# Optimization experiments

Hardware: AMD Instinct MI355X
Metric: run time of the kernel (lower is better)

Reference implementation:

```python
import jax, jax.numpy as jnp
import numpy as np

H = 8            # num_heads
DK = 256         # head_qk_dim
DV = 512         # head_v_dim
EPS = 1e-5
ROPE_BASE = 10000.0


def _rope(x):
    # x: [B, T, H, DK]; GPT-NeoX style (non-interleaved halves), seqlen_offset=0
    B, T, h, d = x.shape
    inv_freq = 1.0 / (ROPE_BASE ** (jnp.arange(0, d, 2, dtype=jnp.float32) / d))  # [d/2]
    t = jnp.arange(T, dtype=jnp.float32)
    freqs = t[:, None] * inv_freq[None, :]              # [T, d/2]
    cos = jnp.cos(freqs)[None, :, None, :]              # [1, T, 1, d/2]
    sin = jnp.sin(freqs)[None, :, None, :]
    x1, x2 = x[..., : d // 2], x[..., d // 2 :]
    return jnp.concatenate([x1 * cos - x2 * sin, x2 * cos + x1 * sin], axis=-1)


def setup_inputs() -> dict:
    key = jax.random.key(0)
    ks = jax.random.split(key, 7)
    hidden = 2048
    B, T = 2, 2048
    w = 0.02
    return {
        "hidden_states": jax.random.normal(ks[0], (B, T, hidden), jnp.float32),
        "Wq": jax.random.normal(ks[1], (hidden, H * DK), jnp.float32) * w,
        "Wk": jax.random.normal(ks[2], (hidden, H * DK), jnp.float32) * w,
        "Wv": jax.random.normal(ks[3], (hidden, H * DV), jnp.float32) * w,
        "Wg": jax.random.normal(ks[4], (hidden, H * DV), jnp.float32) * w,
        "Wo": jax.random.normal(ks[5], (H * DV, hidden), jnp.float32) * w,
        "g_norm_weight": jnp.ones((DV,), jnp.float32),
    }


def reference(hidden_states, Wq, Wk, Wv, Wg, Wo, g_norm_weight):
    B, T, _ = hidden_states.shape
    q = (hidden_states @ Wq).reshape(B, T, H, DK)
    k = (hidden_states @ Wk).reshape(B, T, H, DK)
    v = (hidden_states @ Wv).reshape(B, T, H, DV)
    g = (hidden_states @ Wg).reshape(B, T, H, DV)

    q = _rope(q)
    k = _rope(k)

    # per-head RetNet decay: gamma_h = 1 - 2^(-5-h)
    gamma = 1.0 - jnp.exp2(-5.0 - jnp.arange(H, dtype=jnp.float32))     # [H]
    idx = jnp.arange(T)
    diff = idx[:, None] - idx[None, :]                                   # [T, T]
    causal = diff >= 0
    log2g = jnp.log2(gamma)[:, None, None]                               # [H,1,1]
    D = jnp.where(causal[None], jnp.exp2(log2g * jnp.where(causal, diff, 0)[None]), 0.0)  # [H,T,T]

    scale = DK ** -0.5
    scores = jnp.einsum("bihd,bjhd->bhij", q * scale, k) * D[None]       # [B,H,T,T]
    o = jnp.einsum("bhij,bjhd->bihd", scores, v)                          # [B,T,H,DV]

    # fused RMSNorm (per head over DV) + swish gate
    rms = jax.lax.rsqrt(jnp.mean(o * o, axis=-1, keepdims=True) + EPS)
    o = o * rms * g_norm_weight
    o = o * (g * jax.nn.sigmoid(g))

    return o.reshape(B, T, H * DV) @ Wo
```

## Files before the change

### kernel.cpp

```cpp
#include <hip/hip_runtime.h>
#include <hip/hip_bf16.h>
#include <math.h>

#define NH 8
#define DKk 256
#define DVv 512
#define Bn 2
#define Tn 2048
#define HID 2048
#define EPSf 1e-5f

typedef __bf16 bf16x8 __attribute__((ext_vector_type(8)));
typedef float f32x4 __attribute__((ext_vector_type(4)));
typedef unsigned short us8 __attribute__((ext_vector_type(8)));
using bf16 = __hip_bfloat16;
typedef unsigned short ushort_t;

__device__ __forceinline__ void gload_lds16(const void* g, void* lds_base) {
  __builtin_amdgcn_global_load_lds(
      (const __attribute__((address_space(1))) void*)g,
      (__attribute__((address_space(3))) void*)lds_base, 16, 0, 0);
}

__device__ __forceinline__ ushort_t f2bf_raw(float f) {
  bf16 h = __float2bfloat16(f);
  return *reinterpret_cast<ushort_t*>(&h);
}
__device__ __forceinline__ float bf2f_raw(ushort_t u) {
  union { unsigned int i; float f; } v; v.i = ((unsigned int)u) << 16; return v.f;
}

__global__ void k_f32_to_bf16(const float4* __restrict__ in, ushort4* __restrict__ out, int n4) {
  int i = blockIdx.x * blockDim.x + threadIdx.x;
  if (i >= n4) return;
  float4 v = in[i];
  ushort4 o;
  o.x = f2bf_raw(v.x); o.y = f2bf_raw(v.y); o.z = f2bf_raw(v.z); o.w = f2bf_raw(v.w);
  out[i] = o;
}

__global__ void k_add2_f32(const float4* __restrict__ a, const float4* __restrict__ b,
                           float4* __restrict__ o, int n4) {
  int i = blockIdx.x * blockDim.x + threadIdx.x;
  if (i >= n4) return;
  float4 x = a[i], y = b[i];
  float4 r; r.x = x.x + y.x; r.y = x.y + y.y; r.z = x.z + y.z; r.w = x.w + y.w;
  o[i] = r;
}

__global__ __launch_bounds__(256) void k_transpose64(const float* __restrict__ W, bf16* __restrict__ WT,
                                                     int K, int N) {
  __shared__ unsigned int t32[64 * 33];
  const int tid = threadIdx.x;
  const int n0 = blockIdx.x * 64, k0 = blockIdx.y * 64;
  const int a = tid >> 3;
  const int bq = tid & 7;

  const float* r0 = W + (size_t)(k0 + 2 * a) * N + n0 + bq * 8;
  const float* r1 = r0 + N;
  float4 v00 = *(const float4*)r0;
  float4 v01 = *(const float4*)(r0 + 4);
  float4 v10 = *(const float4*)r1;
  float4 v11 = *(const float4*)(r1 + 4);
  float e0[8] = {v00.x, v00.y, v00.z, v00.w, v01.x, v01.y, v01.z, v01.w};
  float e1[8] = {v10.x, v10.y, v10.z, v10.w, v11.x, v11.y, v11.z, v11.w};
#pragma unroll
  for (int j = 0; j < 8; j++) {
    unsigned int val = (unsigned int)f2bf_raw(e0[j]) | ((unsigned int)f2bf_raw(e1[j]) << 16);
    t32[(bq * 8 + j) * 33 + a] = val;
  }
  __syncthreads();
  const int nl = tid >> 2, part = tid & 3;
  unsigned int c[8];
#pragma unroll
  for (int i = 0; i < 8; i++) c[i] = t32[nl * 33 + part * 8 + i];
  char* dst = (char*)(WT + (size_t)(n0 + nl) * K + k0 + part * 16);
  uint4 lo; lo.x = c[0]; lo.y = c[1]; lo.z = c[2]; lo.w = c[3];
  uint4 hi; hi.x = c[4]; hi.y = c[5]; hi.z = c[6]; hi.w = c[7];
  *(uint4*)dst = lo;
  *(uint4*)(dst + 16) = hi;
}

#define BARX() asm volatile("s_barrier" ::: "memory")
#define LGKM0() { asm volatile("s_waitcnt lgkmcnt(0)" ::: "memory"); __builtin_amdgcn_sched_barrier(0); }
#define VMW4() asm volatile("s_waitcnt vmcnt(4)" ::: "memory")
#define VMW0() asm volatile("s_waitcnt vmcnt(0)" ::: "memory")
#define PRIO1 __builtin_amdgcn_s_setprio(1)
#define PRIO0 __builtin_amdgcn_s_setprio(0)

#define QUADQ(MB, NB)                                                              \
  { _Pragma("unroll") for (int kk_ = 0; kk_ < 2; ++kk_)                            \
    _Pragma("unroll") for (int mf_ = 0; mf_ < 4; ++mf_)                            \
    _Pragma("unroll") for (int nf_ = 0; nf_ < 2; ++nf_)                            \
      acc[(MB) + mf_][(NB) + nf_] = __builtin_amdgcn_mfma_f32_16x16x32_bf16(       \
          ar[(MB) + mf_][kk_], br[(NB) + nf_][kk_],                                \
          acc[(MB) + mf_][(NB) + nf_], 0, 0, 0); }

template <int MODE>
__global__ __launch_bounds__(512, 2) void k_gemm8(const bf16* __restrict__ A, const bf16* __restrict__ BT,
                                                  void* __restrict__ O0, void* __restrict__ O1,
                                                  int nsplit, int M, int Ntot, int Kloop, int Kstride) {
  extern __shared__ char lds[];
  const int tid = threadIdx.x;
  const int lane = tid & 63;
  const int w = tid >> 6;
  const int wr = w >> 2;
  const int wc = w & 3;
  const int quad = lane >> 4, c16 = lane & 15;
  const int m0 = blockIdx.y * 256, n0 = blockIdx.x * 256;
  const int ks = blockIdx.z;

  const bf16* Ab = A + (size_t)ks * Kloop;
  const bf16* Bb = BT + (size_t)ks * Kloop;

  const int srow = (w << 4) | (lane >> 3);
  const int gsw = (((lane & 7) ^ (lane >> 3)) << 4);
  const size_t rowBytes = (size_t)Kstride * 2;
  const char* aS = (const char*)(Ab + (size_t)(m0 + srow) * Kstride) + gsw;
  const char* bS = (const char*)(Bb + (size_t)(n0 + srow) * Kstride) + gsw;

  auto stage = [&](int matB, int buf, int h, int t) {
    const char* base = (matB ? bS : aS) + (size_t)h * 128 * rowBytes + (size_t)t * 128;
    char* ldst = lds + buf * 65536 + matB * 32768 + h * 16384 + w * 2048;
    gload_lds16(base, ldst);
    gload_lds16(base + 8 * rowBytes, ldst + 1024);
  };
  auto ldA = [&](int buf, int mf, int kk) -> bf16x8 {
    int row = wr * 128 + mf * 16 + c16;
    return *(const bf16x8*)(lds + buf * 65536 + row * 128 + ((((kk << 2) | quad) ^ (c16 & 7)) << 4));
  };
  auto ldB = [&](int buf, int nf, int kk) -> bf16x8 {
    int row = wc * 64 + nf * 16 + c16;
    return *(const bf16x8*)(lds + buf * 65536 + 32768 + row * 128 + ((((kk << 2) | quad) ^ (c16 & 7)) << 4));
  };

  f32x4 acc[8][4];
  const f32x4 fz = {0.f, 0.f, 0.f, 0.f};
#pragma unroll
  for (int i = 0; i < 8; i++)
#pragma unroll
    for (int j = 0; j < 4; j++) acc[i][j] = fz;
  bf16x8 ar[8][2], br[4][2];

  const int nT = Kloop >> 6;
  const int nIter = nT >> 1;

  stage(0, 0, 0, 0); stage(0, 0, 1, 0);
  stage(1, 0, 0, 0); stage(1, 0, 1, 0);
  stage(0, 1, 0, 1); stage(0, 1, 1, 1);
  VMW4();
  BARX();

  for (int it = 0; it < nIter; ++it) {
    const int t = it * 2;
    const bool last = (it == nIter - 1);
#pragma unroll
    for (int mf = 0; mf < 4; ++mf) { ar[mf][0] = ldA(0, mf, 0); ar[mf][1] = ldA(0, mf, 1); }
#pragma unroll
    for (int nf = 0; nf < 2; ++nf) { br[nf][0] = ldB(0, nf, 0); br[nf][1] = ldB(0, nf, 1); }
    stage(1, 1, 0, t + 1);
    BARX(); LGKM0();
    PRIO1; QUADQ(0, 0); PRIO0;
    BARX();
#pragma unroll
    for (int mf = 4; mf < 8; ++mf) { ar[mf][0] = ldA(0, mf, 0); ar[mf][1] = ldA(0, mf, 1); }
    stage(1, 1, 1, t + 1);
    BARX(); LGKM0();
    PRIO1; QUADQ(4, 0); PRIO0;
    BARX();
#pragma unroll
    for (int nf = 2; nf < 4; ++nf) { br[nf][0] = ldB(0, nf, 0); br[nf][1] = ldB(0, nf, 1); }
    if (!last) stage(0, 0, 0, t + 2);
    BARX(); LGKM0();
    PRIO1; QUADQ(0, 2); PRIO0;
    BARX();
    if (!last) stage(0, 0, 1, t + 2);
    BARX();
    PRIO1; QUADQ(4, 2); PRIO0;
    if (!last) { VMW4(); } else { VMW0(); }
    BARX();
#pragma unroll
    for (int mf = 0; mf < 4; ++mf) { ar[mf][0] = ldA(1, mf, 0); ar[mf][1] = ldA(1, mf, 1); }
#pragma unroll
    for (int nf = 0; nf < 2; ++nf) { br[nf][0] = ldB(1, nf, 0); br[nf][1] = ldB(1, nf, 1); }
    if (!last) stage(1, 0, 0, t + 2);
    BARX(); LGKM0();
    PRIO1; QUADQ(0, 0); PRIO0;
    BARX();
#pragma unroll
    for (int mf = 4; mf < 8; ++mf) { ar[mf][0] = ldA(1, mf, 0); ar[mf][1] = ldA(1, mf, 1); }
    if (!last) stage(1, 0, 1, t + 2);
    BARX(); LGKM0();
    PRIO1; QUADQ(4, 0); PRIO0;
    BARX();
#pragma unroll
    for (int nf = 2; nf < 4; ++nf) { br[nf][0] = ldB(1, nf, 0); br[nf][1] = ldB(1, nf, 1); }
    if (!last) stage(0, 1, 0, t + 3);
    BARX(); LGKM0();
    PRIO1; QUADQ(0, 2); PRIO0;
    BARX();
    if (!last) stage(0, 1, 1, t + 3);
    BARX();
    PRIO1; QUADQ(4, 2); PRIO0;
    if (!last) VMW4();
    BARX();
  }

  if (MODE == 2) {
    __syncthreads();
    ushort_t* tile = (ushort_t*)lds;
#pragma unroll
    for (int mf = 0; mf < 8; ++mf)
#pragma unroll
      for (int nf = 0; nf < 4; ++nf)
#pragma unroll
        for (int rr = 0; rr < 4; ++rr) {
          int row = wr * 128 + mf * 16 + quad * 4 + rr;
          int col = wc * 64 + nf * 16 + c16;
          tile[row * 256 + col] = f2bf_raw(acc[mf][nf][rr]);
        }
    __syncthreads();
    const bool qside = (n0 < nsplit);
    bf16* Ob = (bf16*)(qside ? O0 : O1);
    const float scale = qside ? 0.0625f : 1.0f;
    const int h = (qside ? n0 : n0 - nsplit) >> 8;
#pragma unroll
    for (int j = 0; j < 8; ++j) {
      int u = j * 512 + tid;
      int row = u >> 4;
      int ch = u & 15;
      const ushort_t* lp = tile + row * 256 + ch * 8;
      us8 lo = *(const us8*)lp;
      us8 hi = *(const us8*)(lp + 128);
      int m = m0 + row;
      float tf = (float)(m & (Tn - 1));
      us8 olo, ohi;
#pragma unroll
      for (int e = 0; e < 8; ++e) {
        int i = ch * 8 + e;
        float inv = exp2f(-(float)i * (13.287712379549449f / 128.0f));
        float ang = tf * inv;
        float s, c;
        sincosf(ang, &s, &c);
        float x1 = bf2f_raw(lo[e]);
        float x2 = bf2f_raw(hi[e]);
        olo[e] = f2bf_raw((x1 * c - x2 * s) * scale);
        ohi[e] = f2bf_raw((x2 * c + x1 * s) * scale);
      }
      ushort_t* dst = (ushort_t*)Ob + ((size_t)m * NH + h) * DKk + ch * 8;
      *(us8*)dst = olo;
      *(us8*)(dst + 128) = ohi;
    }
  } else if (MODE == 1) {
    float* Ob = (float*)(ks ? O1 : O0);
#pragma unroll
    for (int mf = 0; mf < 8; ++mf)
#pragma unroll
      for (int nf = 0; nf < 4; ++nf)
#pragma unroll
        for (int rr = 0; rr < 4; ++rr) {
          int m = m0 + wr * 128 + mf * 16 + quad * 4 + rr;
          int n = n0 + wc * 64 + nf * 16 + c16;
          Ob[(size_t)m * Ntot + n] = acc[mf][nf][rr];
        }
  } else if (MODE == 3 && n0 < nsplit) {
    __syncthreads();
    ushort_t* tile = (ushort_t*)lds;
#pragma unroll
    for (int mf = 0; mf < 8; ++mf)
#pragma unroll
      for (int nf = 0; nf < 4; ++nf)
#pragma unroll
        for (int rr = 0; rr < 4; ++rr) {
          int row = wr * 128 + mf * 16 + quad * 4 + rr;
          int col = wc * 64 + nf * 16 + c16;
          tile[row * 256 + col] = f2bf_raw(acc[mf][nf][rr]);
        }
    __syncthreads();
    const int b = m0 >> 11;
    const int kt0 = (m0 & 2047) >> 5;
    const int h = n0 >> 9;
    const int dv0 = n0 & 511;
    const int bh = b * 8 + h;
    ushort_t* vSo = (ushort_t*)O0;
#pragma unroll
    for (int uu = 0; uu < 16; ++uu) {
      int u = uu * 512 + tid;
      int ktl = u >> 10;
      int chunk = (u >> 8) & 3;
      int dvl = u & 255;
      us8 o;
#pragma unroll
      for (int jj = 0; jj < 8; ++jj)
        o[jj] = tile[(ktl * 32 + chunk * 8 + jj) * 256 + dvl];
      *(us8*)(vSo + ((size_t)(bh * 64 + kt0 + ktl) * 2048 + chunk * 512 + (dv0 + dvl)) * 8) = o;
    }
  } else {
    bf16* Ob; int ldo, nc0;
    if (n0 < nsplit) { Ob = (bf16*)O0; ldo = nsplit; nc0 = n0; }
    else             { Ob = (bf16*)O1; ldo = Ntot - nsplit; nc0 = n0 - nsplit; }
#pragma unroll
    for (int mf = 0; mf < 8; ++mf)
#pragma unroll
      for (int nf = 0; nf < 4; ++nf)
#pragma unroll
        for (int rr = 0; rr < 4; ++rr) {
          int m = m0 + wr * 128 + mf * 16 + quad * 4 + rr;
          int n = nc0 + wc * 64 + nf * 16 + c16;
          Ob[(size_t)m * ldo + n] = __float2bfloat16(acc[mf][nf][rr]);
        }
  }
}

__global__ __launch_bounds__(256, 2) void k_retention(const bf16* __restrict__ q, const bf16* __restrict__ k,
                                                      const char* __restrict__ vS, const bf16* __restrict__ g,
                                                      const float* __restrict__ gnw, bf16* __restrict__ X) {
  extern __shared__ char smem[];
  ushort_t* p_lds_base = (ushort_t*)(smem + 65536);
  float* red = (float*)(smem + 75776);
  bf16* o_lds = (bf16*)smem;

  const int tid = threadIdx.x;
  const int l = tid & 63, w = tid >> 6;
  const int quad = l >> 4, c16 = l & 15;

  const int bid = blockIdx.x;
  const int u = (bid & 255) >> 4;
  const int qt = (bid < 256) ? (31 - u) : u;
  const int bh = bid & 15;
  const int b = bh >> 3, h = bh & 7;
  const int q0 = qt * 64;

  bf16x8 qf[8];
  {
    const bf16* qrow = q + ((size_t)(b * Tn + q0 + w * 16 + c16) * NH + h) * DKk + quad * 8;
#pragma unroll
    for (int c = 0; c < 8; c++) qf[c] = *(const bf16x8*)(qrow + c * 32);
  }

  const float log2g = log2f(1.0f - exp2f(-5.0f - (float)h));

  f32x4 acc[4][8];
  const f32x4 fz = {0.f, 0.f, 0.f, 0.f};
#pragma unroll
  for (int rt = 0; rt < 4; rt++)
#pragma unroll
    for (int n = 0; n < 8; n++) acc[rt][n] = fz;

  const int ktmax = 2 * qt + 1;
  const float Dcut = 30.0f / (-log2g);
  int kt0 = (int)fmaxf(0.0f, floorf(((float)q0 - Dcut) * (1.0f / 32.0f)));

  const char* vS_tilebase = vS + (size_t)(bh * 64) * 32768;

  auto stageK = [&](int kt) {
    const int pb = (kt - kt0) & 1;
#pragma unroll
    for (int i = 0; i < 4; i++) {
      int instr = w * 4 + i;
      int j = instr * 2 + (l >> 5);
      int cg = (l & 31) ^ (j & 7);
      const char* gp = (const char*)(k + ((size_t)(b * Tn + kt * 32 + j) * NH + h) * DKk) + cg * 16;
      gload_lds16(gp, smem + pb * 16384 + instr * 1024);
    }
  };
  auto stageV = [&](int kt) {
#pragma unroll
    for (int i = 0; i < 8; i++) {
      int instr = w * 8 + i;
      const char* gp = vS_tilebase + (size_t)kt * 32768 + instr * 1024 + l * 16;
      gload_lds16(gp, smem + 32768 + instr * 1024);
    }
  };

  auto S_phase = [&](int kt) {
    const int pb = (kt - kt0) & 1;
    f32x4 sacc[2] = {fz, fz};
#pragma unroll
    for (int jt = 0; jt < 2; jt++)
#pragma unroll
      for (int c = 0; c < 8; c++) {
        const char* kp = smem + pb * 16384 + (jt * 16 + c16) * 512 + (((c * 4 + quad) ^ (c16 & 7)) * 16);
        bf16x8 bfrag = *(const bf16x8*)kp;
        sacc[jt] = __builtin_amdgcn_mfma_f32_16x16x32_bf16(qf[c], bfrag, sacc[jt], 0, 0, 0);
      }
    ushort_t* pbuf = p_lds_base + pb * 2560;
#pragma unroll
    for (int jt = 0; jt < 2; jt++)
#pragma unroll
      for (int r = 0; r < 4; r++) {
        int ig = q0 + w * 16 + quad * 4 + r;
        int jg = kt * 32 + jt * 16 + c16;
        int d = ig - jg;
        float val = (d >= 0) ? sacc[jt][r] * exp2f(log2g * (float)d) : 0.0f;
        pbuf[(w * 16 + quad * 4 + r) * 40 + jt * 16 + c16] = f2bf_raw(val);
      }
  };

  auto PV_phase = [&](int kt) {
    const int pb = (kt - kt0) & 1;
    const char* pbuf = (const char*)(p_lds_base + pb * 2560);
    bf16x8 pa[4];
#pragma unroll
    for (int rt = 0; rt < 4; rt++)
      pa[rt] = *(const bf16x8*)(pbuf + (rt * 16 + c16) * 80 + quad * 16);
    const char* v_lds = smem + 32768;
#pragma unroll
    for (int n = 0; n < 8; n++) {
      bf16x8 bv = *(const bf16x8*)(v_lds + quad * 8192 + (w * 128 + n * 16 + c16) * 16);
#pragma unroll
      for (int rt = 0; rt < 4; rt++)
        acc[rt][n] = __builtin_amdgcn_mfma_f32_16x16x32_bf16(pa[rt], bv, acc[rt][n], 0, 0, 0);
    }
  };

#define SBARR() { __builtin_amdgcn_sched_barrier(0); __builtin_amdgcn_s_barrier(); }
#define WLGKM0() { asm volatile("s_waitcnt lgkmcnt(0)" ::: "memory"); }

  stageK(kt0);
  stageV(kt0);
  asm volatile("s_waitcnt vmcnt(8)" ::: "memory");
  SBARR();
  S_phase(kt0);
  if (kt0 + 1 <= ktmax) stageK(kt0 + 1);
  WLGKM0(); SBARR();

  for (int kt = kt0 + 1; kt <= ktmax; ++kt) {
    asm volatile("s_waitcnt vmcnt(4)" ::: "memory");
    SBARR();
    PV_phase(kt - 1);
    WLGKM0(); SBARR();
    stageV(kt);
    asm volatile("s_waitcnt vmcnt(8)" ::: "memory");
    SBARR();
    S_phase(kt);
    if (kt + 1 <= ktmax) stageK(kt + 1);
    WLGKM0(); SBARR();
  }

  asm volatile("s_waitcnt vmcnt(0)" ::: "memory");
  SBARR();
  PV_phase(ktmax);

  __syncthreads();
#pragma unroll
  for (int rt = 0; rt < 4; rt++)
#pragma unroll
    for (int r = 0; r < 4; r++) {
      float s = 0.f;
#pragma unroll
      for (int n = 0; n < 8; n++) { float v = acc[rt][n][r]; s += v * v; }
      s += __shfl_xor(s, 1);
      s += __shfl_xor(s, 2);
      s += __shfl_xor(s, 4);
      s += __shfl_xor(s, 8);
      if (c16 == 0) red[(rt * 16 + quad * 4 + r) * 4 + w] = s;
    }
  __syncthreads();
  float ss[4][4];
#pragma unroll
  for (int rt = 0; rt < 4; rt++)
#pragma unroll
    for (int r = 0; r < 4; r++) {
      int row = rt * 16 + quad * 4 + r;
      float tot = red[row * 4] + red[row * 4 + 1] + red[row * 4 + 2] + red[row * 4 + 3];
      ss[rt][r] = rsqrtf(tot * (1.0f / DVv) + EPSf);
    }
  __syncthreads();

#pragma unroll
  for (int n = 0; n < 8; n++) {
    int col = w * 128 + n * 16 + c16;
    float gw = gnw[col];
#pragma unroll
    for (int rt = 0; rt < 4; rt++)
#pragma unroll
      for (int r = 0; r < 4; r++) {
        int row = rt * 16 + quad * 4 + r;
        o_lds[row * 512 + col] = __float2bfloat16(acc[rt][n][r] * ss[rt][r] * gw);
      }
  }
  __syncthreads();

#pragma unroll
  for (int it = 0; it < 16; it++) {
    int cid = it * 256 + tid;
    int row = cid >> 6;
    int cp = (cid & 63) * 8;
    const ushort_t* gp = (const ushort_t*)g + ((size_t)(b * Tn + q0 + row) * NH + h) * DVv + cp;
    us8 gv = *(const us8*)gp;
    us8 ov;
#pragma unroll
    for (int e = 0; e < 8; e++) {
      float gf = bf2f_raw(gv[e]);
      float gate = gf / (1.0f + expf(-gf));
      float of = __bfloat162float(o_lds[row * 512 + cp + e]);
      ov[e] = f2bf_raw(of * gate);
    }
    *(us8*)((ushort_t*)X + ((size_t)(b * Tn + q0 + row) * NH + h) * DVv + cp) = ov;
  }
}

extern "C" void kernel_launch(void* const* d_in, const int* in_sizes, int n_in,
                              void* d_out, int out_size, void* d_ws, size_t ws_size,
                              hipStream_t stream) {
  const float* hs  = (const float*)d_in[0];
  const float* Wq  = (const float*)d_in[1];
  const float* Wk  = (const float*)d_in[2];
  const float* Wv  = (const float*)d_in[3];
  const float* Wg  = (const float*)d_in[4];
  const float* Wo  = (const float*)d_in[5];
  const float* gnw = (const float*)d_in[6];
  float* out = (float*)d_out;
  char* ws = (char*)d_ws;

  bf16* hsb = (bf16*)(ws);
  bf16* WqT = (bf16*)(ws + 16777216);
  bf16* WkT = (bf16*)(ws + 25165824);
  bf16* WvT = (bf16*)(ws + 33554432);
  bf16* WgT = (bf16*)(ws + 50331648);
  bf16* qb  = (bf16*)(ws + 67108864);
  bf16* kb  = (bf16*)(ws + 83886080);
  char* vSb = ws + 100663296;
  bf16* gb  = (bf16*)(ws + 134217728);
  bf16* WoT = (bf16*)(ws + 33554432);
  bf16* Xb  = (bf16*)ws;
  float* p0 = (float*)(ws + 50331648);
  float* p1 = (float*)(ws + 83886080);

  static bool attr_done = false;
  if (!attr_done) {
    hipFuncSetAttribute((const void*)k_gemm8<1>, hipFuncAttributeMaxDynamicSharedMemorySize, 131072);
    hipFuncSetAttribute((const void*)k_gemm8<2>, hipFuncAttributeMaxDynamicSharedMemorySize, 131072);
    hipFuncSetAttribute((const void*)k_gemm8<3>, hipFuncAttributeMaxDynamicSharedMemorySize, 131072);
    hipFuncSetAttribute((const void*)k_retention, hipFuncAttributeMaxDynamicSharedMemorySize, 76800);
    attr_done = true;
  }

  k_f32_to_bf16<<<8192, 256, 0, stream>>>((const float4*)hs, (ushort4*)hsb, 2097152);
  k_transpose64<<<dim3(HID / 64, HID / 64), 256, 0, stream>>>(Wq, WqT, HID, HID);
  k_transpose64<<<dim3(HID / 64, HID / 64), 256, 0, stream>>>(Wk, WkT, HID, HID);
  k_transpose64<<<dim3(NH * DVv / 64, HID / 64), 256, 0, stream>>>(Wv, WvT, HID, NH * DVv);
  k_transpose64<<<dim3(NH * DVv / 64, HID / 64), 256, 0, stream>>>(Wg, WgT, HID, NH * DVv);
  k_gemm8<2><<<dim3(16, 16), 512, 131072, stream>>>(hsb, WqT, qb, kb, 2048, 4096, 4096, 2048, 2048);
  k_gemm8<3><<<dim3(32, 16), 512, 131072, stream>>>(hsb, WvT, vSb, gb, 4096, 4096, 8192, 2048, 2048);
  k_transpose64<<<dim3(HID / 64, NH * DVv / 64), 256, 0, stream>>>(Wo, WoT, NH * DVv, HID);
  k_retention<<<512, 256, 76800, stream>>>(qb, kb, vSb, gb, gnw, Xb);
  k_gemm8<1><<<dim3(8, 16, 2), 512, 131072, stream>>>(Xb, WoT, p0, p1, 2048, 4096, 2048, 2048, 4096);
  k_add2_f32<<<8192, 256, 0, stream>>>((const float4*)p0, (const float4*)p1, (float4*)out, 2097152);
}
```

Before: 580.1 us.

## Fuse preprocessing kernels and merge Q/K/V/G projections into one GEMM launch

Combines the hidden-state bf16 conversion and all five weight transposes into one k_prep launch. It also merges the separate QK and VG projection GEMMs into one 48x16-block GEMM, with an epilogue that branches by column range to apply RoPE, write the V layout, or store G. The goal is to cut launch overhead and the tail/underfill gaps between small kernels, giving one larger grid for better CU utilization. WoT moves to its own workspace region so it no longer aliases WvT. The merged GEMM relies on WqT/WkT/WvT/WgT being contiguous in the workspace; they are, so one B-operand pointer spans all of them.

Result: faster. 565.3 us (-2.6%).

```diff
diff --git a/kernel.cpp b/kernel.cpp
--- a/kernel.cpp
+++ b/kernel.cpp
@@ -30,15 +30,6 @@
   union { unsigned int i; float f; } v; v.i = ((unsigned int)u) << 16; return v.f;
 }
 
-__global__ void k_f32_to_bf16(const float4* __restrict__ in, ushort4* __restrict__ out, int n4) {
-  int i = blockIdx.x * blockDim.x + threadIdx.x;
-  if (i >= n4) return;
-  float4 v = in[i];
-  ushort4 o;
-  o.x = f2bf_raw(v.x); o.y = f2bf_raw(v.y); o.z = f2bf_raw(v.z); o.w = f2bf_raw(v.w);
-  out[i] = o;
-}
-
 __global__ void k_add2_f32(const float4* __restrict__ a, const float4* __restrict__ b,
                            float4* __restrict__ o, int n4) {
   int i = blockIdx.x * blockDim.x + threadIdx.x;
@@ -48,11 +39,10 @@
   o[i] = r;
 }
 
-__global__ __launch_bounds__(256) void k_transpose64(const float* __restrict__ W, bf16* __restrict__ WT,
-                                                     int K, int N) {
-  __shared__ unsigned int t32[64 * 33];
-  const int tid = threadIdx.x;
-  const int n0 = blockIdx.x * 64, k0 = blockIdx.y * 64;
+__device__ __forceinline__ void transpose64_body(const float* __restrict__ W, bf16* __restrict__ WT,
+                                                 int K, int N, int bx, int by, int tid,
+                                                 unsigned int* t32 ) {
+  const int n0 = bx * 64, k0 = by * 64;
   const int a = tid >> 3;
   const int bq = tid & 7;
 
@@ -81,6 +71,32 @@
   *(uint4*)(dst + 16) = hi;
 }
 
+__global__ __launch_bounds__(256) void k_prep(const float* __restrict__ hs, ushort4* __restrict__ hsb4,
+                                              const float* __restrict__ Wq, const float* __restrict__ Wk,
+                                              const float* __restrict__ Wv, const float* __restrict__ Wg,
+                                              const float* __restrict__ Wo,
+                                              bf16* __restrict__ WqT, bf16* __restrict__ WkT,
+                                              bf16* __restrict__ WvT, bf16* __restrict__ WgT,
+                                              bf16* __restrict__ WoT) {
+  __shared__ unsigned int t32[64 * 33];
+  const int bid = blockIdx.x;
+  const int tid = threadIdx.x;
+  if (bid < 8192) {
+    int i = bid * 256 + tid;
+    float4 v = ((const float4*)hs)[i];
+    ushort4 o;
+    o.x = f2bf_raw(v.x); o.y = f2bf_raw(v.y); o.z = f2bf_raw(v.z); o.w = f2bf_raw(v.w);
+    hsb4[i] = o;
+    return;
+  }
+  int t = bid - 8192;
+  if (t < 1024)      transpose64_body(Wq, WqT, HID, HID, t & 31, t >> 5, tid, t32);
+  else if (t < 2048) { t -= 1024; transpose64_body(Wk, WkT, HID, HID, t & 31, t >> 5, tid, t32); }
+  else if (t < 4096) { t -= 2048; transpose64_body(Wv, WvT, HID, NH * DVv, t & 63, t >> 6, tid, t32); }
+  else if (t < 6144) { t -= 4096; transpose64_body(Wg, WgT, HID, NH * DVv, t & 63, t >> 6, tid, t32); }
+  else               { t -= 6144; transpose64_body(Wo, WoT, NH * DVv, HID, t & 31, t >> 5, tid, t32); }
+}
+
 #define BARX() asm volatile("s_barrier" ::: "memory")
 #define LGKM0() { asm volatile("s_waitcnt lgkmcnt(0)" ::: "memory"); __builtin_amdgcn_sched_barrier(0); }
 #define VMW4() asm volatile("s_waitcnt vmcnt(4)" ::: "memory")
@@ -99,6 +115,7 @@
 template <int MODE>
 __global__ __launch_bounds__(512, 2) void k_gemm8(const bf16* __restrict__ A, const bf16* __restrict__ BT,
                                                   void* __restrict__ O0, void* __restrict__ O1,
+                                                  void* __restrict__ O2, void* __restrict__ O3,
                                                   int nsplit, int M, int Ntot, int Kloop, int Kstride) {
   extern __shared__ char lds[];
   const int tid = threadIdx.x;
@@ -206,50 +223,98 @@
     BARX();
   }
 
-  if (MODE == 2) {
-    __syncthreads();
-    ushort_t* tile = (ushort_t*)lds;
-#pragma unroll
-    for (int mf = 0; mf < 8; ++mf)
-#pragma unroll
-      for (int nf = 0; nf < 4; ++nf)
-#pragma unroll
-        for (int rr = 0; rr < 4; ++rr) {
-          int row = wr * 128 + mf * 16 + quad * 4 + rr;
-          int col = wc * 64 + nf * 16 + c16;
-          tile[row * 256 + col] = f2bf_raw(acc[mf][nf][rr]);
+  if (MODE == 4) {
+    if (n0 < 4096) {
+      __syncthreads();
+      ushort_t* tile = (ushort_t*)lds;
+#pragma unroll
+      for (int mf = 0; mf < 8; ++mf)
+#pragma unroll
+        for (int nf = 0; nf < 4; ++nf)
+#pragma unroll
+          for (int rr = 0; rr < 4; ++rr) {
+            int row = wr * 128 + mf * 16 + quad * 4 + rr;
+            int col = wc * 64 + nf * 16 + c16;
+            tile[row * 256 + col] = f2bf_raw(acc[mf][nf][rr]);
+          }
+      __syncthreads();
+      const bool qside = (n0 < 2048);
+      bf16* Ob = (bf16*)(qside ? O0 : O1);
+      const float scale = qside ? 0.0625f : 1.0f;
+      const int h = (qside ? n0 : n0 - 2048) >> 8;
+#pragma unroll
+      for (int j = 0; j < 8; ++j) {
+        int u = j * 512 + tid;
+        int row = u >> 4;
+        int ch = u & 15;
+        const ushort_t* lp = tile + row * 256 + ch * 8;
+        us8 lo = *(const us8*)lp;
+        us8 hi = *(const us8*)(lp + 128);
+        int m = m0 + row;
+        float tf = (float)(m & (Tn - 1));
+        us8 olo, ohi;
+#pragma unroll
+        for (int e = 0; e < 8; ++e) {
+          int i = ch * 8 + e;
+          float inv = exp2f(-(float)i * (13.287712379549449f / 128.0f));
+          float ang = tf * inv;
+          float s, c;
+          sincosf(ang, &s, &c);
+          float x1 = bf2f_raw(lo[e]);
+          float x2 = bf2f_raw(hi[e]);
+          olo[e] = f2bf_raw((x1 * c - x2 * s) * scale);
+          ohi[e] = f2bf_raw((x2 * c + x1 * s) * scale);
         }
-    __syncthreads();
-    const bool qside = (n0 < nsplit);
-    bf16* Ob = (bf16*)(qside ? O0 : O1);
-    const float scale = qside ? 0.0625f : 1.0f;
-    const int h = (qside ? n0 : n0 - nsplit) >> 8;
-#pragma unroll
-    for (int j = 0; j < 8; ++j) {
-      int u = j * 512 + tid;
-      int row = u >> 4;
-      int ch = u & 15;
-      const ushort_t* lp = tile + row * 256 + ch * 8;
-      us8 lo = *(const us8*)lp;
-      us8 hi = *(const us8*)(lp + 128);
-      int m = m0 + row;
-      float tf = (float)(m & (Tn - 1));
-      us8 olo, ohi;
-#pragma unroll
-      for (int e = 0; e < 8; ++e) {
-        int i = ch * 8 + e;
-        float inv = exp2f(-(float)i * (13.287712379549449f / 128.0f));
-        float ang = tf * inv;
-        float s, c;
-        sincosf(ang, &s, &c);
-        float x1 = bf2f_raw(lo[e]);
-        float x2 = bf2f_raw(hi[e]);
-        olo[e] = f2bf_raw((x1 * c - x2 * s) * scale);
-        ohi[e] = f2bf_raw((x2 * c + x1 * s) * scale);
+        ushort_t* dst = (ushort_t*)Ob + ((size_t)m * NH + h) * DKk + ch * 8;
+        *(us8*)dst = olo;
+        *(us8*)(dst + 128) = ohi;
       }
-      ushort_t* dst = (ushort_t*)Ob + ((size_t)m * NH + h) * DKk + ch * 8;
-      *(us8*)dst = olo;
-      *(us8*)(dst + 128) = ohi;
+    } else if (n0 < 8192) {
+      __syncthreads();
+      ushort_t* tile = (ushort_t*)lds;
+#pragma unroll
+      for (int mf = 0; mf < 8; ++mf)
+#pragma unroll
+        for (int nf = 0; nf < 4; ++nf)
+#pragma unroll
+          for (int rr = 0; rr < 4; ++rr) {
+            int row = wr * 128 + mf * 16 + quad * 4 + rr;
+            int col = wc * 64 + nf * 16 + c16;
+            tile[row * 256 + col] = f2bf_raw(acc[mf][nf][rr]);
+          }
+      __syncthreads();
+      const int nv = n0 - 4096;
+      const int b = m0 >> 11;
+      const int kt0 = (m0 & 2047) >> 5;
+      const int h = nv >> 9;
+      const int dv0 = nv & 511;
+      const int bh = b * 8 + h;
+      ushort_t* vSo = (ushort_t*)O2;
+#pragma unroll
+      for (int uu = 0; uu < 16; ++uu) {
+        int u = uu * 512 + tid;
+        int ktl = u >> 10;
+        int chunk = (u >> 8) & 3;
+        int dvl = u & 255;
+        us8 o;
+#pragma unroll
+        for (int jj = 0; jj < 8; ++jj)
+          o[jj] = tile[(ktl * 32 + chunk * 8 + jj) * 256 + dvl];
+        *(us8*)(vSo + ((size_t)(bh * 64 + kt0 + ktl) * 2048 + chunk * 512 + (dv0 + dvl)) * 8) = o;
+      }
+    } else {
+      bf16* Ob = (bf16*)O3;
+      const int nc0 = n0 - 8192;
+#pragma unroll
+      for (int mf = 0; mf < 8; ++mf)
+#pragma unroll
+        for (int nf = 0; nf < 4; ++nf)
+#pragma unroll
+          for (int rr = 0; rr < 4; ++rr) {
+            int m = m0 + wr * 128 + mf * 16 + quad * 4 + rr;
+            int n = nc0 + wc * 64 + nf * 16 + c16;
+            Ob[(size_t)m * 4096 + n] = __float2bfloat16(acc[mf][nf][rr]);
+          }
     }
   } else if (MODE == 1) {
     float* Ob = (float*)(ks ? O1 : O0);
@@ -262,52 +327,6 @@
           int m = m0 + wr * 128 + mf * 16 + quad * 4 + rr;
           int n = n0 + wc * 64 + nf * 16 + c16;
           Ob[(size_t)m * Ntot + n] = acc[mf][nf][rr];
-        }
-  } else if (MODE == 3 && n0 < nsplit) {
-    __syncthreads();
-    ushort_t* tile = (ushort_t*)lds;
-#pragma unroll
-    for (int mf = 0; mf < 8; ++mf)
-#pragma unroll
-      for (int nf = 0; nf < 4; ++nf)
-#pragma unroll
-        for (int rr = 0; rr < 4; ++rr) {
-          int row = wr * 128 + mf * 16 + quad * 4 + rr;
-          int col = wc * 64 + nf * 16 + c16;
-          tile[row * 256 + col] = f2bf_raw(acc[mf][nf][rr]);
-        }
-    __syncthreads();
-    const int b = m0 >> 11;
-    const int kt0 = (m0 & 2047) >> 5;
-    const int h = n0 >> 9;
-    const int dv0 = n0 & 511;
-    const int bh = b * 8 + h;
-    ushort_t* vSo = (ushort_t*)O0;
-#pragma unroll
-    for (int uu = 0; uu < 16; ++uu) {
-      int u = uu * 512 + tid;
-      int ktl = u >> 10;
-      int chunk = (u >> 8) & 3;
-      int dvl = u & 255;
-      us8 o;
-#pragma unroll
-      for (int jj = 0; jj < 8; ++jj)
-        o[jj] = tile[(ktl * 32 + chunk * 8 + jj) * 256 + dvl];
-      *(us8*)(vSo + ((size_t)(bh * 64 + kt0 + ktl) * 2048 + chunk * 512 + (dv0 + dvl)) * 8) = o;
-    }
-  } else {
-    bf16* Ob; int ldo, nc0;
-    if (n0 < nsplit) { Ob = (bf16*)O0; ldo = nsplit; nc0 = n0; }
-    else             { Ob = (bf16*)O1; ldo = Ntot - nsplit; nc0 = n0 - nsplit; }
-#pragma unroll
-    for (int mf = 0; mf < 8; ++mf)
-#pragma unroll
-      for (int nf = 0; nf < 4; ++nf)
-#pragma unroll
-        for (int rr = 0; rr < 4; ++rr) {
-          int m = m0 + wr * 128 + mf * 16 + quad * 4 + rr;
-          int n = nc0 + wc * 64 + nf * 16 + c16;
-          Ob[(size_t)m * ldo + n] = __float2bfloat16(acc[mf][nf][rr]);
         }
   }
 }
@@ -523,7 +542,7 @@
   bf16* kb  = (bf16*)(ws + 83886080);
   char* vSb = ws + 100663296;
   bf16* gb  = (bf16*)(ws + 134217728);
-  bf16* WoT = (bf16*)(ws + 33554432);
+  bf16* WoT = (bf16*)(ws + 167772160);
   bf16* Xb  = (bf16*)ws;
   float* p0 = (float*)(ws + 50331648);
   float* p1 = (float*)(ws + 83886080);
@@ -531,21 +550,17 @@
   static bool attr_done = false;
   if (!attr_done) {
     hipFuncSetAttribute((const void*)k_gemm8<1>, hipFuncAttributeMaxDynamicSharedMemorySize, 131072);
-    hipFuncSetAttribute((const void*)k_gemm8<2>, hipFuncAttributeMaxDynamicSharedMemorySize, 131072);
-    hipFuncSetAttribute((const void*)k_gemm8<3>, hipFuncAttributeMaxDynamicSharedMemorySize, 131072);
+    hipFuncSetAttribute((const void*)k_gemm8<4>, hipFuncAttributeMaxDynamicSharedMemorySize, 131072);
     hipFuncSetAttribute((const void*)k_retention, hipFuncAttributeMaxDynamicSharedMemorySize, 76800);
     attr_done = true;
   }
 
-  k_f32_to_bf16<<<8192, 256, 0, stream>>>((const float4*)hs, (ushort4*)hsb, 2097152);
-  k_transpose64<<<dim3(HID / 64, HID / 64), 256, 0, stream>>>(Wq, WqT, HID, HID);
-  k_transpose64<<<dim3(HID / 64, HID / 64), 256, 0, stream>>>(Wk, WkT, HID, HID);
-  k_transpose64<<<dim3(NH * DVv / 64, HID / 64), 256, 0, stream>>>(Wv, WvT, HID, NH * DVv);
-  k_transpose64<<<dim3(NH * DVv / 64, HID / 64), 256, 0, stream>>>(Wg, WgT, HID, NH * DVv);
-  k_gemm8<2><<<dim3(16, 16), 512, 131072, stream>>>(hsb, WqT, qb, kb, 2048, 4096, 4096, 2048, 2048);
-  k_gemm8<3><<<dim3(32, 16), 512, 131072, stream>>>(hsb, WvT, vSb, gb, 4096, 4096, 8192, 2048, 2048);
-  k_transpose64<<<dim3(HID / 64, NH * DVv / 64), 256, 0, stream>>>(Wo, WoT, NH * DVv, HID);
+  k_prep<<<16384, 256, 0, stream>>>(hs, (ushort4*)hsb, Wq, Wk, Wv, Wg, Wo,
+                                    WqT, WkT, WvT, WgT, WoT);
+  k_gemm8<4><<<dim3(48, 16), 512, 131072, stream>>>(hsb, WqT, qb, kb, vSb, gb,
+                                                    0, 4096, 12288, 2048, 2048);
   k_retention<<<512, 256, 76800, stream>>>(qb, kb, vSb, gb, gnw, Xb);
-  k_gemm8<1><<<dim3(8, 16, 2), 512, 131072, stream>>>(Xb, WoT, p0, p1, 2048, 4096, 2048, 2048, 4096);
+  k_gemm8<1><<<dim3(8, 16, 2), 512, 131072, stream>>>(Xb, WoT, p0, p1, nullptr, nullptr,
+                                                      2048, 4096, 2048, 2048, 4096);
   k_add2_f32<<<8192, 256, 0, stream>>>((const float4*)p0, (const float4*)p1, (float4*)out, 2097152);
 }
```
